# Optimization experiments

Hardware: AMD Instinct MI355X
Metric: run time of the kernel (lower is better)

Reference implementation:

```python
import jax, jax.numpy as jnp
import numpy as np

VOCAB = 100277
EMBED = 32
B, S = 8, 512


def setup_inputs() -> dict:
    key = jax.random.key(0)
    k1, k2, k3, k4 = jax.random.split(key, 4)
    input_seq = jax.random.randint(k1, (B, S), 0, VOCAB, dtype=jnp.int64)
    predictions = jax.random.randint(k2, (B, S), 0, VOCAB, dtype=jnp.int64)
    emb = jax.random.normal(k3, (VOCAB, EMBED), dtype=jnp.float32)
    # torch Linear default init scale ~ 1/sqrt(fan_in); keep simple gaussian scaled
    W = jax.random.normal(k4, (VOCAB, EMBED), dtype=jnp.float32) * (1.0 / np.sqrt(EMBED))
    b = jnp.zeros((VOCAB,), dtype=jnp.float32)
    return {"input_seq": input_seq, "predictions": predictions, "emb": emb, "W": W, "b": b}


def reference(input_seq, predictions, emb, W, b):
    # embedding lookup: [B,S,E]
    embeds = emb[input_seq]
    # linear projection to vocab: [B,S,V]
    logits = jnp.einsum('bse,ve->bsv', embeds, W) + b
    n, v = B * S, VOCAB
    logits_flat = logits.reshape(n, v)
    targets = predictions.reshape(n)
    # mean cross-entropy (stable log_softmax, single pass)
    logp = jax.nn.log_softmax(logits_flat, axis=-1)
    nll = -jnp.take_along_axis(logp, targets[:, None], axis=-1)[:, 0]
    loss = jnp.mean(nll)
    return (logits_flat, loss)
```

## Files before the change

### kernel.cpp

```cpp
#include <hip/hip_runtime.h>
#include <cstddef>
#include <cstdint>


using f32x4 = __attribute__((ext_vector_type(4))) float;
using f16x8 = __attribute__((ext_vector_type(8))) _Float16;

constexpr int N_ROWS  = 4096;
constexpr int ROWS_PB = 16;
constexpr int NBLK    = N_ROWS / ROWS_PB;
constexpr int WIN     = 1024;
constexpr int NWIN    = 98;
constexpr int TPB     = 1024;
constexpr int WAVES   = 16;
constexpr int TILES   = 4;
constexpr int V_TILES = NWIN * (WIN / 16);
constexpr int TSTR    = 1028;

constexpr size_t RS_OFF = 0;
constexpr size_t EF_OFF = 64 * 1024;
constexpr size_t EF_BYTES = (size_t)NBLK * 64 * 16;
constexpr size_t WF_OFF = EF_OFF + EF_BYTES;

static __device__ __forceinline__ uint4 pack8h(const float* f) {
    unsigned short u[8];
#pragma unroll
    for (int i = 0; i < 8; ++i) {
        _Float16 h = (_Float16)f[i];
        u[i] = __builtin_bit_cast(unsigned short, h);
    }
    uint4 r;
    r.x = (unsigned)u[0] | ((unsigned)u[1] << 16);
    r.y = (unsigned)u[2] | ((unsigned)u[3] << 16);
    r.z = (unsigned)u[4] | ((unsigned)u[5] << 16);
    r.w = (unsigned)u[6] | ((unsigned)u[7] << 16);
    return r;
}

__global__ __launch_bounds__(256) void prep_wfrag(
    const float* __restrict__ W, uint4* __restrict__ Wf, int V)
{
    const int g    = blockIdx.x * 256 + threadIdx.x;
    const int lane = g & 63;
    const int tile = g >> 6;
    int col = tile * 16 + (lane & 15);
    if (col >= V) col = V - 1;
    const int k0 = (lane >> 4) * 8;
    const float* wp = W + (size_t)col * 32 + k0;
    float f[8];
    *reinterpret_cast<float4*>(f)     = *reinterpret_cast<const float4*>(wp);
    *reinterpret_cast<float4*>(f + 4) = *reinterpret_cast<const float4*>(wp + 4);
    Wf[g] = pack8h(f);
}

__global__ __launch_bounds__(256) void prep_efrag(
    const int* __restrict__ seq, const float* __restrict__ emb,
    uint4* __restrict__ Ef)
{
    const int g    = blockIdx.x * 256 + threadIdx.x;
    const int lane = g & 63;
    const int c    = g >> 6;
    const int row  = c * 16 + (lane & 15);
    const int k0   = (lane >> 4) * 8;
    const int idx  = seq[row];
    const float* ep = emb + (size_t)idx * 32 + k0;
    float f[8];
    *reinterpret_cast<float4*>(f)     = *reinterpret_cast<const float4*>(ep);
    *reinterpret_cast<float4*>(f + 4) = *reinterpret_cast<const float4*>(ep + 4);
    Ef[g] = pack8h(f);
}

__global__ __launch_bounds__(TPB) void bigram_main(
    const uint4* __restrict__ Wf,
    const float* __restrict__ bias,
    const uint4* __restrict__ Ef,
    float*       __restrict__ logits,
    float*       __restrict__ rowsum,
    int V)
{
    __shared__ float buf[ROWS_PB][TSTR];
    __shared__ float lsum[WAVES][ROWS_PB];

    const int tid  = threadIdx.x;
    const int lane = tid & 63;
    const int wid  = tid >> 6;
    const int lgrp = lane >> 4;
    const int lcol = lane & 15;
    const int b    = blockIdx.x;

    const f16x8 E = __builtin_bit_cast(f16x8, Ef[(size_t)b * 64 + lane]);
    const int wcol = wid * (TILES * 16);
    float rs = 0.f;

    uint4 Wc[TILES]; f32x4 Bc[TILES];
#pragma unroll
    for (int t = 0; t < TILES; ++t) {
        Wc[t] = Wf[(size_t)(wid * TILES + t) * 64 + lane];
        const float4 b4 = *reinterpret_cast<const float4*>(
            bias + wcol + t * 16 + lgrp * 4);
        Bc[t] = f32x4{b4.x, b4.y, b4.z, b4.w};
    }

    for (int s = 0; s < NWIN; ++s) {
        const int  cbase = s * WIN;
        const bool last  = (s == NWIN - 1);

        const int  sp    = (s + 1 < NWIN) ? s + 1 : s;
        const bool ptail = (sp == NWIN - 1);
        uint4 Wn[TILES]; f32x4 Bn[TILES];
#pragma unroll
        for (int t = 0; t < TILES; ++t)
            Wn[t] = Wf[(size_t)(sp * (WIN / 16) + wid * TILES + t) * 64 + lane];
#pragma unroll
        for (int t = 0; t < TILES; ++t) {
            const int c0 = sp * WIN + wcol + t * 16 + lgrp * 4;
            if (!ptail) {
                const float4 b4 = *reinterpret_cast<const float4*>(bias + c0);
                Bn[t] = f32x4{b4.x, b4.y, b4.z, b4.w};
            } else {
#pragma unroll
                for (int j = 0; j < 4; ++j) {
                    const int c = c0 + j;
                    Bn[t][j] = bias[c < V ? c : V - 1];
                }
            }
        }

#pragma unroll
        for (int t = 0; t < TILES; ++t) {
            const f32x4 acc = __builtin_amdgcn_mfma_f32_16x16x32_f16(
                __builtin_bit_cast(f16x8, Wc[t]), E, Bc[t], 0, 0, 0);
            if (!last) {
                rs += __expf(acc[0]) + __expf(acc[1]) +
                      __expf(acc[2]) + __expf(acc[3]);
            } else {
                const int c0 = cbase + wcol + t * 16 + lgrp * 4;
#pragma unroll
                for (int j = 0; j < 4; ++j)
                    if (c0 + j < V) rs += __expf(acc[j]);
            }
            *reinterpret_cast<f32x4*>(&buf[lcol][wcol + t * 16 + lgrp * 4]) = acc;
        }

        asm volatile("s_waitcnt lgkmcnt(0)" ::: "memory");
        __builtin_amdgcn_s_barrier();
        __builtin_amdgcn_sched_barrier(0);

        {
            const int n = b * ROWS_PB + wid;
            float* dst = logits + (size_t)n * V + cbase;
#pragma unroll
            for (int i = 0; i < 4; ++i) {
                const int colL = i * 256 + lane * 4;
                const f32x4 v = *reinterpret_cast<const f32x4*>(&buf[wid][colL]);
                if (!last) {
                    __builtin_nontemporal_store(v, reinterpret_cast<f32x4*>(dst + colL));
                } else {
                    const int cg = cbase + colL;
                    if (cg + 3 < V) {
                        __builtin_nontemporal_store(v, reinterpret_cast<f32x4*>(dst + colL));
                    } else {
#pragma unroll
                        for (int j = 0; j < 4; ++j)
                            if (cg + j < V)
                                __builtin_nontemporal_store(v[j], dst + colL + j);
                    }
                }
            }
        }

        asm volatile("s_waitcnt lgkmcnt(0)" ::: "memory");
        __builtin_amdgcn_s_barrier();
        __builtin_amdgcn_sched_barrier(0);

#pragma unroll
        for (int t = 0; t < TILES; ++t) { Wc[t] = Wn[t]; Bc[t] = Bn[t]; }
    }

    rs += __shfl_xor(rs, 16, 64);
    rs += __shfl_xor(rs, 32, 64);
    if (lane < 16) lsum[wid][lcol] = rs;
    __syncthreads();
    if (tid < ROWS_PB) {
        float t = 0.f;
#pragma unroll
        for (int w = 0; w < WAVES; ++w) t += lsum[w][tid];
        rowsum[b * ROWS_PB + tid] = t;
    }
}

__global__ void bigram_loss(
    const int*   __restrict__ seq,
    const int*   __restrict__ pred,
    const float* __restrict__ emb,
    const float* __restrict__ W,
    const float* __restrict__ bias,
    const float* __restrict__ rowsum,
    float*       __restrict__ loss,
    int N)
{
    const int tid = threadIdx.x;
    float local = 0.f;
    for (int n = blockIdx.x * blockDim.x + tid; n < N; n += gridDim.x * blockDim.x) {
        const int r = seq[n], t = pred[n];
        const float4* e4 = reinterpret_cast<const float4*>(emb + (size_t)r * 32);
        const float4* w4 = reinterpret_cast<const float4*>(W + (size_t)t * 32);
        float d = bias[t];
#pragma unroll
        for (int i = 0; i < 8; ++i) {
            const float4 e = e4[i], w = w4[i];
            d += e.x * w.x + e.y * w.y + e.z * w.z + e.w * w.w;
        }
        local += __logf(rowsum[n]) - d;
    }
#pragma unroll
    for (int off = 32; off >= 1; off >>= 1) local += __shfl_xor(local, off, 64);
    __shared__ float r4[4];
    if ((tid & 63) == 0) r4[tid >> 6] = local;
    __syncthreads();
    if (tid == 0) {
        const float s = r4[0] + r4[1] + r4[2] + r4[3];
        atomicAdd(loss, s / (float)N);
    }
}

extern "C" void kernel_launch(void* const* d_in, const int* in_sizes, int n_in,
                              void* d_out, int out_size, void* d_ws, size_t ws_size,
                              hipStream_t stream)
{
    const int*   seq  = (const int*)d_in[0];
    const int*   pred = (const int*)d_in[1];
    const float* emb  = (const float*)d_in[2];
    const float* W    = (const float*)d_in[3];
    const float* bias = (const float*)d_in[4];

    const int N = in_sizes[0];
    const int V = in_sizes[4];

    float* logits = (float*)d_out;
    float* loss   = logits + (size_t)N * V;

    char*  ws     = (char*)d_ws;
    float* rowsum = (float*)(ws + RS_OFF);
    uint4* Ef     = (uint4*)(ws + EF_OFF);
    uint4* Wf     = (uint4*)(ws + WF_OFF);

    hipMemsetAsync((void*)loss, 0, sizeof(float), stream);

    hipLaunchKernelGGL(prep_wfrag, dim3(V_TILES * 64 / 256), dim3(256), 0, stream,
                       W, Wf, V);
    hipLaunchKernelGGL(prep_efrag, dim3(NBLK * 64 / 256), dim3(256), 0, stream,
                       seq, emb, Ef);

    hipLaunchKernelGGL(bigram_main, dim3(NBLK), dim3(TPB), 0, stream,
                       Wf, bias, Ef, logits, rowsum, V);

    hipLaunchKernelGGL(bigram_loss, dim3(16), dim3(256), 0, stream,
                       seq, pred, emb, W, bias, rowsum, loss, N);
}
```

Before: 428.3 us.

## Realign logits row stores via shifted LDS carry buffer and merge prep kernels

```diff
diff --git a/kernel.cpp b/kernel.cpp
--- a/kernel.cpp
+++ b/kernel.cpp
@@ -15,7 +15,7 @@
 constexpr int WAVES   = 16;
 constexpr int TILES   = 4;
 constexpr int V_TILES = NWIN * (WIN / 16);
-constexpr int TSTR    = 1028;
+constexpr int PSTR    = 64 + WIN + 4;
 
 constexpr size_t RS_OFF = 0;
 constexpr size_t EF_OFF = 64 * 1024;
@@ -37,37 +37,39 @@
     return r;
 }
 
-__global__ __launch_bounds__(256) void prep_wfrag(
-    const float* __restrict__ W, uint4* __restrict__ Wf, int V)
-{
-    const int g    = blockIdx.x * 256 + threadIdx.x;
-    const int lane = g & 63;
-    const int tile = g >> 6;
-    int col = tile * 16 + (lane & 15);
-    if (col >= V) col = V - 1;
-    const int k0 = (lane >> 4) * 8;
-    const float* wp = W + (size_t)col * 32 + k0;
-    float f[8];
-    *reinterpret_cast<float4*>(f)     = *reinterpret_cast<const float4*>(wp);
-    *reinterpret_cast<float4*>(f + 4) = *reinterpret_cast<const float4*>(wp + 4);
-    Wf[g] = pack8h(f);
-}
-
-__global__ __launch_bounds__(256) void prep_efrag(
-    const int* __restrict__ seq, const float* __restrict__ emb,
-    uint4* __restrict__ Ef)
-{
-    const int g    = blockIdx.x * 256 + threadIdx.x;
-    const int lane = g & 63;
-    const int c    = g >> 6;
-    const int row  = c * 16 + (lane & 15);
-    const int k0   = (lane >> 4) * 8;
-    const int idx  = seq[row];
-    const float* ep = emb + (size_t)idx * 32 + k0;
-    float f[8];
-    *reinterpret_cast<float4*>(f)     = *reinterpret_cast<const float4*>(ep);
-    *reinterpret_cast<float4*>(f + 4) = *reinterpret_cast<const float4*>(ep + 4);
-    Ef[g] = pack8h(f);
+__global__ __launch_bounds__(256) void prep_frags(
+    const float* __restrict__ W,
+    const int*   __restrict__ seq,
+    const float* __restrict__ emb,
+    uint4* __restrict__ Wf,
+    uint4* __restrict__ Ef,
+    int V)
+{
+    const int g = blockIdx.x * 256 + threadIdx.x;
+    if (g < V_TILES * 64) {
+        const int lane = g & 63;
+        const int tile = g >> 6;
+        int col = tile * 16 + (lane & 15);
+        if (col >= V) col = V - 1;
+        const int k0 = (lane >> 4) * 8;
+        const float* wp = W + (size_t)col * 32 + k0;
+        float f[8];
+        *reinterpret_cast<float4*>(f)     = *reinterpret_cast<const float4*>(wp);
+        *reinterpret_cast<float4*>(f + 4) = *reinterpret_cast<const float4*>(wp + 4);
+        Wf[g] = pack8h(f);
+    } else {
+        const int g2   = g - V_TILES * 64;
+        const int lane = g2 & 63;
+        const int c    = g2 >> 6;
+        const int row  = c * 16 + (lane & 15);
+        const int k0   = (lane >> 4) * 8;
+        const int idx  = seq[row];
+        const float* ep = emb + (size_t)idx * 32 + k0;
+        float f[8];
+        *reinterpret_cast<float4*>(f)     = *reinterpret_cast<const float4*>(ep);
+        *reinterpret_cast<float4*>(f + 4) = *reinterpret_cast<const float4*>(ep + 4);
+        Ef[g2] = pack8h(f);
+    }
 }
 
 __global__ __launch_bounds__(TPB) void bigram_main(
@@ -78,7 +80,7 @@
     float*       __restrict__ rowsum,
     int V)
 {
-    __shared__ float buf[ROWS_PB][TSTR];
+    __shared__ float ebuf[ROWS_PB][PSTR];
     __shared__ float lsum[WAVES][ROWS_PB];
 
     const int tid  = threadIdx.x;
@@ -91,6 +93,10 @@
     const f16x8 E = __builtin_bit_cast(f16x8, Ef[(size_t)b * 64 + lane]);
     const int wcol = wid * (TILES * 16);
     float rs = 0.f;
+
+    const int n_row = b * ROWS_PB + wid;
+    const int Lsh   = (21 * n_row) & 31;
+    float* rowbase  = logits + (size_t)n_row * V;
 
     uint4 Wc[TILES]; f32x4 Bc[TILES];
 #pragma unroll
@@ -139,7 +145,7 @@
                 for (int j = 0; j < 4; ++j)
                     if (c0 + j < V) rs += __expf(acc[j]);
             }
-            *reinterpret_cast<f32x4*>(&buf[lcol][wcol + t * 16 + lgrp * 4]) = acc;
+            *reinterpret_cast<f32x4*>(&ebuf[lcol][64 + wcol + t * 16 + lgrp * 4]) = acc;
         }
 
         asm volatile("s_waitcnt lgkmcnt(0)" ::: "memory");
@@ -147,25 +153,44 @@
         __builtin_amdgcn_sched_barrier(0);
 
         {
-            const int n = b * ROWS_PB + wid;
-            float* dst = logits + (size_t)n * V + cbase;
+            const int slotCur = (s & 1) * 32;
 #pragma unroll
             for (int i = 0; i < 4; ++i) {
                 const int colL = i * 256 + lane * 4;
-                const f32x4 v = *reinterpret_cast<const f32x4*>(&buf[wid][colL]);
-                if (!last) {
-                    __builtin_nontemporal_store(v, reinterpret_cast<f32x4*>(dst + colL));
+                float v[4];
+                if (i == 0) {
+#pragma unroll
+                    for (int j = 0; j < 4; ++j) {
+                        const int idx = colL + j;
+                        int a = 64 + idx - Lsh;
+                        if (idx < Lsh && slotCur == 0) a -= 32;
+                        v[j] = ebuf[wid][a];
+                    }
                 } else {
-                    const int cg = cbase + colL;
-                    if (cg + 3 < V) {
-                        __builtin_nontemporal_store(v, reinterpret_cast<f32x4*>(dst + colL));
-                    } else {
-#pragma unroll
-                        for (int j = 0; j < 4; ++j)
-                            if (cg + j < V)
-                                __builtin_nontemporal_store(v[j], dst + colL + j);
-                    }
+#pragma unroll
+                    for (int j = 0; j < 4; ++j)
+                        v[j] = ebuf[wid][64 + colL + j - Lsh];
                 }
+                const int gcol = cbase - Lsh + colL;
+                if (s == 0 && i == 0) {
+#pragma unroll
+                    for (int j = 0; j < 4; ++j)
+                        if (gcol + j >= 0)
+                            __builtin_nontemporal_store(v[j], rowbase + gcol + j);
+                } else if (last && i == 3) {
+#pragma unroll
+                    for (int j = 0; j < 4; ++j)
+                        if (gcol + j < V)
+                            __builtin_nontemporal_store(v[j], rowbase + gcol + j);
+                } else {
+                    __builtin_nontemporal_store(
+                        f32x4{v[0], v[1], v[2], v[3]},
+                        reinterpret_cast<f32x4*>(rowbase + gcol));
+                }
+            }
+            if (lane < 32) {
+                const float cv = ebuf[wid][64 + WIN - 32 + lane];
+                ebuf[wid][((s + 1) & 1) * 32 + lane] = cv;
             }
         }
 
@@ -189,7 +214,7 @@
     }
 }
 
-__global__ void bigram_loss(
+__global__ __launch_bounds__(1024) void bigram_loss(
     const int*   __restrict__ seq,
     const int*   __restrict__ pred,
     const float* __restrict__ emb,
@@ -201,7 +226,7 @@
 {
     const int tid = threadIdx.x;
     float local = 0.f;
-    for (int n = blockIdx.x * blockDim.x + tid; n < N; n += gridDim.x * blockDim.x) {
+    for (int n = tid; n < N; n += 1024) {
         const int r = seq[n], t = pred[n];
         const float4* e4 = reinterpret_cast<const float4*>(emb + (size_t)r * 32);
         const float4* w4 = reinterpret_cast<const float4*>(W + (size_t)t * 32);
@@ -215,12 +240,14 @@
     }
 #pragma unroll
     for (int off = 32; off >= 1; off >>= 1) local += __shfl_xor(local, off, 64);
-    __shared__ float r4[4];
-    if ((tid & 63) == 0) r4[tid >> 6] = local;
+    __shared__ float r16[16];
+    if ((tid & 63) == 0) r16[tid >> 6] = local;
     __syncthreads();
     if (tid == 0) {
-        const float s = r4[0] + r4[1] + r4[2] + r4[3];
-        atomicAdd(loss, s / (float)N);
+        float s = 0.f;
+#pragma unroll
+        for (int w = 0; w < 16; ++w) s += r16[w];
+        loss[0] = s / (float)N;
     }
 }
 
@@ -245,16 +272,13 @@
     uint4* Ef     = (uint4*)(ws + EF_OFF);
     uint4* Wf     = (uint4*)(ws + WF_OFF);
 
-    hipMemsetAsync((void*)loss, 0, sizeof(float), stream);
-
-    hipLaunchKernelGGL(prep_wfrag, dim3(V_TILES * 64 / 256), dim3(256), 0, stream,
-                       W, Wf, V);
-    hipLaunchKernelGGL(prep_efrag, dim3(NBLK * 64 / 256), dim3(256), 0, stream,
-                       seq, emb, Ef);
+    const int prepTotal = V_TILES * 64 + NBLK * 64;
+    hipLaunchKernelGGL(prep_frags, dim3(prepTotal / 256), dim3(256), 0, stream,
+                       W, seq, emb, Wf, Ef, V);
 
     hipLaunchKernelGGL(bigram_main, dim3(NBLK), dim3(TPB), 0, stream,
                        Wf, bias, Ef, logits, rowsum, V);
 
-    hipLaunchKernelGGL(bigram_loss, dim3(16), dim3(256), 0, stream,
+    hipLaunchKernelGGL(bigram_loss, dim3(1), dim3(1024), 0, stream,
                        seq, pred, emb, W, bias, rowsum, loss, N);
 }
```

Result: faster. 392.1 us (-8.4%).
